# Kernel tuning notes

Hardware: AMD Instinct MI355X
Metric: run time of the kernel (lower is better)

Reference implementation:

```python
import jax, jax.numpy as jnp
import numpy as np

B, N, C, H, D, K = 8, 2000, 64, 64, 16, 2  # batch, nodes, hidden, hidden_hidden, embed_dim, cheb_k


def setup_inputs() -> dict:
    key = jax.random.key(0)
    ks = jax.random.split(key, 12)
    f = lambda k, s, sc=1.0: jax.random.normal(k, s, dtype=jnp.float32) * sc
    return {
        "z": f(ks[0], (B, N, C)),
        "W_in": f(ks[1], (H, C), 0.1),
        "b_in": f(ks[2], (H,), 0.1),
        "W_out": f(ks[3], (C * C, H), 0.05),
        "b_out": f(ks[4], (C * C,), 0.05),
        "emb": f(ks[5], (N, D), 0.1),
        "wp": f(ks[6], (D, K, H, H), 0.1),
        "bp": f(ks[7], (D, H), 0.1),
        "w1": f(ks[8], (C,)),
        "w2": f(ks[9], (C,)),
        "vs": f(ks[10], (N, N), 0.02),
        "bs": f(ks[11], (N, N), 0.02),
    }


def reference(z, W_in, b_in, W_out, b_out, emb, wp, bp, w1, w2, vs, bs):
    # linear_in + relu: (B,N,C) -> (B,N,H)
    h = jax.nn.relu(jnp.einsum("bnc,hc->bnh", z, W_in) + b_in)

    # data-adaptive graph: softmax over rows of relu(emb @ emb^T)
    A = jax.nn.softmax(jax.nn.relu(emb @ emb.T), axis=1)  # (N,N)
    S = jnp.stack([jnp.eye(N, dtype=z.dtype), A], axis=0)  # (K,N,N), cheb_k=2

    # spatial attention on h (x = h.unsqueeze(1), f_in == H == C)
    e1 = h @ w1  # (B,N)
    e2 = h @ w2  # (B,N)
    prod = e1[:, :, None] * e2[:, None, :]  # (B,N,N) outer product
    E = jax.nn.softmax(
        jnp.einsum("nm,bmp->bnp", vs, jax.nn.sigmoid(prod + bs)), axis=-1
    )  # (B,N,N)

    # batched supports: E.unsqueeze(1) @ S -> (B,K,N,N)
    sup = jnp.einsum("bnm,kmp->bknp", E, S)

    # node-adaptive weights / bias
    weights = jnp.einsum("nd,dkio->nkio", emb, wp)  # (N,K,H,H)
    bias = emb @ bp  # (N,H)

    # graph conv
    x_g = jnp.einsum("bknm,bmc->bnkc", sup, h)  # (B,N,K,H)
    g = jnp.einsum("bnki,nkio->bno", x_g, weights) + bias  # (B,N,H)

    # linear_out + view + tanh, scaled by 0.1
    out = jnp.tanh(jnp.einsum("bnh,oh->bno", g, W_out) + b_out)
    return 0.1 * out.reshape(B, N, C, C)
```

## Files before the change

kernel.cpp:

```cpp
#include <hip/hip_runtime.h>
#include <hip/hip_bf16.h>

#define NN 2000
#define NP 2048
#define BB 8
#define HH 64
#define DD 16

typedef __hip_bfloat16 bf16;
typedef short bf16x8 __attribute__((ext_vector_type(8)));
typedef float f32x4 __attribute__((ext_vector_type(4)));

__device__ __forceinline__ float fast_sigmoid(float x) {
    return 1.0f / (1.0f + __expf(-x));
}
__device__ __forceinline__ float fast_tanh(float x) {
    float e = __expf(2.0f * x);
    return 1.0f - 2.0f / (e + 1.0f);
}

__device__ __forceinline__ void glds16(const void* g, void* l) {
    __builtin_amdgcn_global_load_lds(
        (const __attribute__((address_space(1))) void*)g,
        (__attribute__((address_space(3))) void*)l, 16, 0, 0);
}

__global__ __launch_bounds__(256) void k_h(
        const float* __restrict__ z, const float* __restrict__ W_in,
        const float* __restrict__ b_in, const float* __restrict__ w1,
        const float* __restrict__ w2, float* __restrict__ h,
        float* __restrict__ e1, float* __restrict__ e2) {
    __shared__ float WT[64 * 65];
    __shared__ float zs[8][64];
    int t = threadIdx.x;
    int lane = t & 63, ty = t >> 6;
    int bn0 = blockIdx.x * 8;
    for (int i = t; i < 64 * 64; i += 256) {
        int hh = i >> 6, c = i & 63;
        WT[c * 65 + hh] = W_in[i];
    }
    #pragma unroll
    for (int q = 0; q < 2; q++) {
        int r = ty * 2 + q;
        zs[r][lane] = z[(size_t)(bn0 + r) * 64 + lane];
    }
    __syncthreads();
    #pragma unroll
    for (int q = 0; q < 2; q++) {
        int r = ty * 2 + q;
        float acc = b_in[lane];
        #pragma unroll
        for (int c = 0; c < 64; c++) acc += zs[r][c] * WT[c * 65 + lane];
        float hv = fmaxf(acc, 0.0f);
        h[(size_t)(bn0 + r) * 64 + lane] = hv;
        float p1 = hv * w1[lane], p2 = hv * w2[lane];
        #pragma unroll
        for (int off = 32; off > 0; off >>= 1) {
            p1 += __shfl_down(p1, off);
            p2 += __shfl_down(p2, off);
        }
        if (lane == 0) { e1[bn0 + r] = p1; e2[bn0 + r] = p2; }
    }
}

__global__ __launch_bounds__(256) void k_mega(
        const float* __restrict__ e1, const float* __restrict__ e2,
        const float* __restrict__ bs, bf16* __restrict__ Tt,
        const float* __restrict__ vs, bf16* __restrict__ vs_bf,
        const float* __restrict__ emb, bf16* __restrict__ A,
        const float* __restrict__ wp, float* __restrict__ Wn_all,
        const float* __restrict__ h, bf16* __restrict__ hTcat,
        bf16* __restrict__ hsT,
        const float* __restrict__ W_out, bf16* __restrict__ Wo_bf) {
    __shared__ float smem[4160];
    int bid = blockIdx.x, t = threadIdx.x;

    if (bid < 1024) {
        int mt = bid & 31, pt = bid >> 5;
        float* tile = smem;
        int tx = t & 63, ty = t >> 6;
        int m0 = mt * 64, p0 = pt * 64;
        for (int i = ty * 16; i < ty * 16 + 16; i++) {
            int m = m0 + i, p = p0 + tx;
            tile[i * 65 + tx] = (m < NN && p < NN) ? bs[(size_t)m * NN + p] : 0.0f;
        }
        __syncthreads();
        int m = m0 + tx;
        for (int b = 0; b < BB; b++) {
            float e1v = (m < NN) ? e1[b * NN + m] : 0.0f;
            bf16* Tb = Tt + (size_t)b * NP * NP;
            for (int i = ty * 16; i < ty * 16 + 16; i++) {
                int p = p0 + i;
                float v = 0.0f;
                if (m < NN && p < NN)
                    v = fast_sigmoid(e1v * e2[b * NN + p] + tile[tx * 65 + i]);
                Tb[((size_t)p) * NP + m] = __float2bfloat16(v);
            }
        }
        return;
    }
    bid -= 1024;
    if (bid < 16384) {
        int id = bid * 256 + t;
        int n = id >> 11, m = id & (NP - 1);
        float v = (n < NN && m < NN) ? vs[n * NN + m] : 0.0f;
        vs_bf[id] = __float2bfloat16(v);
        return;
    }
    bid -= 16384;
    if (bid < 2048) {
        int i = bid;
        if (i >= NN) {
            for (int j = t; j < NP; j += 256) A[(size_t)i * NP + j] = __float2bfloat16(0.0f);
            return;
        }
        float* rowbuf = smem;
        float* red = smem + 2048;
        float* ei = smem + 2304;
        if (t < DD) ei[t] = emb[i * DD + t];
        __syncthreads();
        float lmax = -1e30f;
        for (int j = t; j < NP; j += 256) {
            float s = 0.0f;
            if (j < NN) {
                #pragma unroll
                for (int d = 0; d < DD; d++) s += ei[d] * emb[j * DD + d];
                s = fmaxf(s, 0.0f);
                lmax = fmaxf(lmax, s);
            }
            rowbuf[j] = s;
        }
        red[t] = lmax; __syncthreads();
        for (int o = 128; o > 0; o >>= 1) { if (t < o) red[t] = fmaxf(red[t], red[t + o]); __syncthreads(); }
        float mx = red[0];
        __syncthreads();
        float lsum = 0.0f;
        for (int j = t; j < NN; j += 256) {
            float e = __expf(rowbuf[j] - mx);
            rowbuf[j] = e; lsum += e;
        }
        red[t] = lsum; __syncthreads();
        for (int o = 128; o > 0; o >>= 1) { if (t < o) red[t] += red[t + o]; __syncthreads(); }
        float inv = 1.0f / red[0];
        for (int j = t; j < NP; j += 256)
            A[(size_t)i * NP + j] = __float2bfloat16(j < NN ? rowbuf[j] * inv : 0.0f);
        return;
    }
    bid -= 2048;
    if (bid < 512) {
        float* embs = smem;
        int n0 = (bid & 15) * 128;
        int jo = (bid >> 4) * 256 + t;
        float wv[16];
        #pragma unroll
        for (int d = 0; d < 16; d++) wv[d] = wp[(size_t)d * 8192 + jo];
        for (int s = t; s < 128 * 16; s += 256) {
            int i = s >> 4, d = s & 15;
            int n = n0 + i;
            embs[s] = (n < NN) ? emb[n * 16 + d] : 0.f;
        }
        __syncthreads();
        for (int i = 0; i < 128; i++) {
            int n = n0 + i;
            if (n >= NN) break;
            const f32x4* ev = (const f32x4*)&embs[i * 16];
            f32x4 ea = ev[0], eb = ev[1], ec = ev[2], ed = ev[3];
            float a = 0.f;
            #pragma unroll
            for (int q = 0; q < 4; q++) a += ea[q] * wv[q];
            #pragma unroll
            for (int q = 0; q < 4; q++) a += eb[q] * wv[4 + q];
            #pragma unroll
            for (int q = 0; q < 4; q++) a += ec[q] * wv[8 + q];
            #pragma unroll
            for (int q = 0; q < 4; q++) a += ed[q] * wv[12 + q];
            Wn_all[(size_t)n * 8192 + jo] = a;
        }
        return;
    }
    bid -= 512;
    if (bid < 256) {
        float* tile = smem;
        int nt = bid & 31, b = bid >> 5;
        int tx = t & 63, ty = t >> 6;
        int n0 = nt * 64;
        for (int i = ty * 16; i < ty * 16 + 16; i++) {
            int n = n0 + i;
            tile[i * 65 + tx] = (n < NN) ? h[((size_t)b * NN + n) * 64 + tx] : 0.0f;
        }
        __syncthreads();
        for (int i = ty * 16; i < ty * 16 + 16; i++) {
            bf16 v = __float2bfloat16(tile[tx * 65 + i]);
            hTcat[((size_t)b * 64 + i) * NP + n0 + tx] = v;
            hsT[((size_t)b * 128 + i) * NP + n0 + tx] = v;
        }
        return;
    }
    bid -= 256;
    {
        int id = bid * 256 + t;
        Wo_bf[id] = __float2bfloat16(W_out[id]);
    }
}

__global__ __launch_bounds__(256) void k_redT(const float* __restrict__ AhPart,
                                              bf16* __restrict__ hsT) {
    __shared__ float tile[64 * 65];
    int pt = blockIdx.x, b = blockIdx.y;
    int tx = threadIdx.x & 63, ty = threadIdx.x >> 6;
    int p0 = pt * 64, q0 = b * 64;
    const long long TOT = (long long)NP * 512;
    for (int i = ty * 16; i < ty * 16 + 16; i++) {
        long long base = ((long long)p0 + i) * 512 + q0 + tx;
        float s = AhPart[base];
        #pragma unroll
        for (int sl = 1; sl < 4; sl++) s += AhPart[sl * TOT + base];
        tile[i * 65 + tx] = s;
    }
    __syncthreads();
    for (int i = ty * 16; i < ty * 16 + 16; i++)
        hsT[((size_t)b * 128 + 64 + i) * NP + p0 + tx] =
            __float2bfloat16(tile[tx * 65 + i]);
}

#define MFMA_B16 __builtin_amdgcn_mfma_f32_16x16x32_bf16
#define VM8 asm volatile("s_waitcnt vmcnt(8)" ::: "memory")
#define VM4 asm volatile("s_waitcnt vmcnt(4)" ::: "memory")
#define VM0 asm volatile("s_waitcnt vmcnt(0)" ::: "memory")
#define VMN
#define PHASE(BUF, KH, JP, READA, STAGE, VMS)                                \
  {                                                                          \
    if (READA) {                                                             \
      _Pragma("unroll")                                                      \
      for (int ii = 0; ii < 8; ii++)                                         \
        a[ii] = *(const bf16x8*)(LDSb + (BUF) * 16384 + (KH) * 8192 + aoff[ii]); \
    }                                                                        \
    b[0] = *(const bf16x8*)(LDSb + 32768 + (BUF) * 16384 + (KH) * 8192 + boff[(JP) * 2]); \
    b[1] = *(const bf16x8*)(LDSb + 32768 + (BUF) * 16384 + (KH) * 8192 + boff[(JP) * 2 + 1]); \
    STAGE;                                                                   \
    asm volatile("s_waitcnt lgkmcnt(0)" ::: "memory");                       \
    __builtin_amdgcn_sched_barrier(0);                                       \
    __builtin_amdgcn_s_setprio(1);                                           \
    _Pragma("unroll")                                                        \
    for (int ii = 0; ii < 8; ii++) {                                         \
      acc[ii][(JP) * 2]     = MFMA_B16(a[ii], b[0], acc[ii][(JP) * 2], 0, 0, 0);     \
      acc[ii][(JP) * 2 + 1] = MFMA_B16(a[ii], b[1], acc[ii][(JP) * 2 + 1], 0, 0, 0); \
    }                                                                        \
    __builtin_amdgcn_s_setprio(0);                                           \
    __builtin_amdgcn_sched_barrier(0);                                       \
    VMS;                                                                     \
    __builtin_amdgcn_s_barrier();                                            \
    __builtin_amdgcn_sched_barrier(0);                                       \
  }

__global__ __launch_bounds__(512, 2) void k_gemm256pv(
        const bf16* __restrict__ X, const bf16* __restrict__ Yt,
        const bf16* __restrict__ hsT, float* __restrict__ xgPart,
        float* __restrict__ rsPart,
        int K, int ldx, int ldy, long long sY, long long sHs) {
    __shared__ short LDSb[65536];
    int id = blockIdx.x;
    int xcd = id & 7;
    int bx = (id >> 3) & 7;
    int group = (id >> 6) * 8 + xcd;
    int by = group & 7, z = group >> 3;
    const bf16* Xp = X;
    const bf16* Yp = Yt + (long long)z * sY;
    int tid = threadIdx.x;
    int m0 = bx * 256, n0 = by * 256;
    int wave = tid >> 6, lane = tid & 63;
    int wr = wave >> 2, wc = wave & 3;
    int fr = lane & 15, kq = lane >> 4;

    f32x4 zero = {0.f, 0.f, 0.f, 0.f};
    f32x4 acc[8][4];
    #pragma unroll
    for (int i = 0; i < 8; i++)
        #pragma unroll
        for (int j = 0; j < 4; j++) acc[i][j] = zero;

    auto SR = [&](int isA, int buf, int kh, int tile) {
        int rbase = (isA ? 0 : 32768) + buf * 16384 + kh * 8192;
        long long kb = (long long)tile * 64 + kh * 32;
        #pragma unroll
        for (int q = 0; q < 2; q++) {
            int pos = q * 512 + tid;
            int row = pos >> 2;
            int scol = ((pos & 3) ^ (row & 3) ^ ((row >> 2) & 3)) * 8;
            const bf16* g = (isA ? Xp + (long long)(m0 + row) * ldx
                                 : Yp + (long long)(n0 + row) * ldy) + kb + scol;
            glds16(g, LDSb + rbase + pos * 8);
        }
    };

    int aoff[8], boff[4];
    #pragma unroll
    for (int i = 0; i < 8; i++) {
        int row = wr * 128 + i * 16 + fr;
        aoff[i] = row * 32 + ((kq ^ (row & 3) ^ ((row >> 2) & 3)) << 3);
    }
    #pragma unroll
    for (int j = 0; j < 4; j++) {
        int row = wc * 64 + j * 16 + fr;
        boff[j] = row * 32 + ((kq ^ (row & 3) ^ ((row >> 2) & 3)) << 3);
    }

    bf16x8 a[8], b[2];
    int NITER = K >> 7;

    SR(1, 0, 0, 0); SR(0, 0, 0, 0);
    SR(1, 0, 1, 0); SR(0, 0, 1, 0);
    SR(1, 1, 0, 1); SR(0, 1, 0, 1);
    VM8;
    __builtin_amdgcn_s_barrier();
    __builtin_amdgcn_sched_barrier(0);

    for (int i = 0; i < NITER - 1; i++) {
        int t1 = 2 * i + 1, t2 = 2 * i + 2, t3 = 2 * i + 3;
        PHASE(0, 0, 0, 1, { SR(1, 1, 1, t1); }, VM8)
        PHASE(0, 0, 1, 0, { SR(0, 1, 1, t1); }, VM8)
        PHASE(0, 1, 0, 1, { SR(1, 0, 0, t2); }, VM8)
        PHASE(0, 1, 1, 0, { SR(0, 0, 0, t2); }, VM8)
        PHASE(1, 0, 0, 1, { SR(1, 0, 1, t2); }, VM8)
        PHASE(1, 0, 1, 0, { SR(0, 0, 1, t2); }, VM8)
        PHASE(1, 1, 0, 1, { SR(1, 1, 0, t3); }, VM8)
        PHASE(1, 1, 1, 0, { SR(0, 1, 0, t3); }, VM8)
    }
    {
        int t1 = 2 * NITER - 1;
        PHASE(0, 0, 0, 1, { SR(1, 1, 1, t1); }, VM8)
        PHASE(0, 0, 1, 0, { SR(0, 1, 1, t1); }, VM8)
        PHASE(0, 1, 0, 1, { }, VM8)
        PHASE(0, 1, 1, 0, { }, VM4)
        PHASE(1, 0, 0, 1, { }, VM4)
        PHASE(1, 0, 1, 0, { }, VM0)
        PHASE(1, 1, 0, 1, { }, VMN)
        PHASE(1, 1, 1, 0, { }, VMN)
    }
    __syncthreads();

    int rq = kq * 4;
    #pragma unroll
    for (int i = 0; i < 8; i++) {
        #pragma unroll
        for (int r = 0; r < 4; r++) {
            int lrow = wr * 128 + i * 16 + rq + r;
            float rs = 0.f;
            #pragma unroll
            for (int j = 0; j < 4; j++) {
                int lcol = wc * 64 + j * 16 + fr;
                float e = (n0 + lcol < NN) ? __expf(acc[i][j][r]) : 0.f;
                bf16 bv = __float2bfloat16(e);
                int sl = (lcol >> 3) ^ (lrow & 7);
                LDSb[lrow * 256 + sl * 8 + (lcol & 7)] = *(short*)&bv;
                rs += e;
            }
            rs += __shfl_xor(rs, 1);
            rs += __shfl_xor(rs, 2);
            rs += __shfl_xor(rs, 4);
            rs += __shfl_xor(rs, 8);
            if (fr == 0)
                rsPart[((long long)z * 32 + by * 4 + wc) * NP + m0 + lrow] = rs;
        }
    }
    __syncthreads();

    const bf16* hz = hsT + (long long)z * sHs;
    int wr2 = wave >> 2, wc2 = wave & 3;
    f32x4 acc2[8][2];
    #pragma unroll
    for (int i = 0; i < 8; i++)
        #pragma unroll
        for (int jj = 0; jj < 2; jj++) acc2[i][jj] = zero;
    #pragma unroll
    for (int ks = 0; ks < 8; ks++) {
        bf16x8 a2[8], b2[2];
        #pragma unroll
        for (int i = 0; i < 8; i++) {
            int row = wr2 * 128 + i * 16 + fr;
            int sl = (ks * 4 + kq) ^ (row & 7);
            a2[i] = *(const bf16x8*)(LDSb + row * 256 + sl * 8);
        }
        #pragma unroll
        for (int jj = 0; jj < 2; jj++)
            b2[jj] = *(const bf16x8*)(hz + (long long)(wc2 * 32 + jj * 16 + fr) * NP
                                      + n0 + ks * 32 + kq * 8);
        #pragma unroll
        for (int i = 0; i < 8; i++)
            #pragma unroll
            for (int jj = 0; jj < 2; jj++)
                acc2[i][jj] = MFMA_B16(a2[i], b2[jj], acc2[i][jj], 0, 0, 0);
    }
    #pragma unroll
    for (int i = 0; i < 8; i++)
        #pragma unroll
        for (int jj = 0; jj < 2; jj++) {
            int jcol = wc2 * 32 + jj * 16 + fr;
            #pragma unroll
            for (int r = 0; r < 4; r++) {
                int n = m0 + wr2 * 128 + i * 16 + rq + r;
                xgPart[(long long)n * 8192 + by * 1024 + z * 128 + jcol] = acc2[i][jj][r];
            }
        }
}

template<bool TANH, int KSPLIT>
__global__ __launch_bounds__(256) void k_gemm_bt(
        const bf16* __restrict__ X, const bf16* __restrict__ Yt,
        float* __restrict__ C, const float* __restrict__ bias,
        int K, int ldx, int ldy, int ldc,
        long long sX, long long sY, long long sC, long long sSlice) {
    __shared__ short As[128 * 32];
    __shared__ short Bs[128 * 32];
    int zz = blockIdx.z;
    int ks = 0;
    if (KSPLIT > 1) { ks = zz % KSPLIT; zz /= KSPLIT; }
    const bf16* Xp = X + (long long)zz * sX;
    const bf16* Yp = Yt + (long long)zz * sY;
    float* Cp = C + (long long)zz * sC + (long long)ks * sSlice;
    int tid = threadIdx.x;
    int m0 = blockIdx.x * 128, n0 = blockIdx.y * 128;
    int wave = tid >> 6, lane = tid & 63;
    int wm = (wave >> 1) * 64, wn = (wave & 1) * 64;
    int fr = lane & 15, kq = lane >> 4;

    f32x4 zero = {0.f, 0.f, 0.f, 0.f};
    f32x4 acc[4][4];
    #pragma unroll
    for (int i = 0; i < 4; i++)
        #pragma unroll
        for (int j = 0; j < 4; j++) acc[i][j] = zero;

    int lrow = lane >> 2, lcol = (lane & 3) * 8;
    const bf16* xg0 = Xp + (long long)(m0 + wave * 16 + lrow) * ldx + lcol;
    const bf16* xg1 = xg0 + (long long)64 * ldx;
    const bf16* yg0 = Yp + (long long)(n0 + wave * 16 + lrow) * ldy + lcol;
    const bf16* yg1 = yg0 + (long long)64 * ldy;
    short* lA0 = As + wave * 512;
    short* lA1 = As + (wave + 4) * 512;
    short* lB0 = Bs + wave * 512;
    short* lB1 = Bs + (wave + 4) * 512;

    int kbeg = (KSPLIT > 1) ? ks * (K / KSPLIT) : 0;
    int kend = kbeg + K / KSPLIT;
    for (int k0 = kbeg; k0 < kend; k0 += 32) {
        __syncthreads();
        glds16(xg0 + k0, lA0);
        glds16(xg1 + k0, lA1);
        glds16(yg0 + k0, lB0);
        glds16(yg1 + k0, lB1);
        __syncthreads();
        bf16x8 a[4], b[4];
        #pragma unroll
        for (int i = 0; i < 4; i++)
            a[i] = *(const bf16x8*)(As + (wm + i * 16 + fr) * 32 + kq * 8);
        #pragma unroll
        for (int j = 0; j < 4; j++)
            b[j] = *(const bf16x8*)(Bs + (wn + j * 16 + fr) * 32 + kq * 8);
        #pragma unroll
        for (int i = 0; i < 4; i++)
            #pragma unroll
            for (int j = 0; j < 4; j++)
                acc[i][j] = __builtin_amdgcn_mfma_f32_16x16x32_bf16(a[i], b[j], acc[i][j], 0, 0, 0);
    }
    int rq = kq * 4;
    for (int i = 0; i < 4; i++)
        for (int j = 0; j < 4; j++) {
            int col = n0 + wn + j * 16 + fr;
            float bv = TANH ? bias[col] : 0.0f;
            #pragma unroll
            for (int r = 0; r < 4; r++) {
                int row = m0 + wm + i * 16 + rq + r;
                float v = acc[i][j][r];
                Cp[(long long)row * ldc + col] =
                    TANH ? 0.1f * fast_tanh(v + bv) : v;
            }
        }
}

__global__ __launch_bounds__(256) void k_g(
        const float* __restrict__ Wn_all, const float* __restrict__ bp,
        const float* __restrict__ emb, const float* __restrict__ xgPart,
        const float* __restrict__ rsPart, bf16* __restrict__ gbf) {
    __shared__ float Wn[8192];
    __shared__ float xgs[1024];
    __shared__ float biass[64];
    __shared__ float invs[8];
    __shared__ float rsred[256];
    int n = blockIdx.x, t = threadIdx.x;
    rsred[t] = rsPart[(size_t)t * NP + n];
    if (t >= 64 && t < 128) {
        int o = t - 64;
        float a = 0.f;
        #pragma unroll
        for (int d = 0; d < 16; d++) a += emb[n * 16 + d] * bp[d * 64 + o];
        biass[o] = a;
    }
    {
        const f32x4* src = (const f32x4*)(Wn_all + (size_t)n * 8192);
        f32x4* dst = (f32x4*)Wn;
        #pragma unroll
        for (int s = 0; s < 8; s++) dst[s * 256 + t] = src[s * 256 + t];
    }
    __syncthreads();
    if (t < 8) {
        float s = 0.f;
        #pragma unroll
        for (int y = 0; y < 32; y++) s += rsred[t * 32 + y];
        invs[t] = 1.0f / s;
    }
    __syncthreads();
    for (int s = 0; s < 4; s++) {
        int id = t + s * 256;
        int b = id >> 7, j = id & 127;
        const float* xp = xgPart + (size_t)n * 8192 + b * 128 + j;
        float a = xp[0];
        #pragma unroll
        for (int by = 1; by < 8; by++) a += xp[by * 1024];
        xgs[id] = a * invs[b];
    }
    __syncthreads();
    int o = t & 63, bh = t >> 6;
    for (int half = 0; half < 2; half++) {
        int b = bh + half * 4;
        float a = biass[o];
        for (int j = 0; j < 128; j++) a += xgs[b * 128 + j] * Wn[j * 64 + o];
        gbf[((size_t)b * NN + n) * 64 + o] = __float2bfloat16(a);
    }
}

extern "C" void kernel_launch(void* const* d_in, const int* in_sizes, int n_in,
                              void* d_out, int out_size, void* d_ws, size_t ws_size,
                              hipStream_t stream) {
    const float* z     = (const float*)d_in[0];
    const float* W_in  = (const float*)d_in[1];
    const float* b_in  = (const float*)d_in[2];
    const float* W_out = (const float*)d_in[3];
    const float* b_out = (const float*)d_in[4];
    const float* emb   = (const float*)d_in[5];
    const float* wp    = (const float*)d_in[6];
    const float* bp    = (const float*)d_in[7];
    const float* w1    = (const float*)d_in[8];
    const float* w2    = (const float*)d_in[9];
    const float* vs    = (const float*)d_in[10];
    const float* bs    = (const float*)d_in[11];

    char* p = (char*)d_ws;
    auto alloc = [&](size_t bytes) -> char* {
        char* r = p;
        p += (bytes + 255) & ~(size_t)255;
        return r;
    };
    float* h       = (float*)alloc((size_t)BB * NN * 64 * 4);
    float* e1      = (float*)alloc((size_t)BB * NN * 4);
    float* e2      = (float*)alloc((size_t)BB * NN * 4);
    bf16*  A_bf    = (bf16*) alloc((size_t)NP * NP * 2);
    bf16*  vs_bf   = (bf16*) alloc((size_t)NP * NP * 2);
    bf16*  Tt_all  = (bf16*) alloc((size_t)BB * NP * NP * 2);
    float* rsPart  = (float*)alloc((size_t)BB * 32 * NP * 4);
    bf16*  hTcat   = (bf16*) alloc((size_t)512 * NP * 2);
    float* AhPart  = (float*)alloc((size_t)4 * NP * 512 * 4);
    bf16*  hsT     = (bf16*) alloc((size_t)BB * 128 * NP * 2);
    float* xgPart  = (float*)alloc((size_t)NP * 8192 * 4);
    bf16*  gbf     = (bf16*) alloc((size_t)BB * NN * 64 * 2);
    bf16*  Wo_bf   = (bf16*) alloc((size_t)4096 * 64 * 2);
    float* Wn_all  = (float*)alloc((size_t)NN * 8192 * 4);

    k_h<<<BB * NN / 8, 256, 0, stream>>>(z, W_in, b_in, w1, w2, h, e1, e2);

    k_mega<<<1024 + 16384 + 2048 + 512 + 256 + 1024, 256, 0, stream>>>(
        e1, e2, bs, Tt_all, vs, vs_bf, emb, A_bf, wp, Wn_all,
        h, hTcat, hsT, W_out, Wo_bf);

    k_gemm_bt<false, 4><<<dim3(16, 4, 4), 256, 0, stream>>>(
        A_bf, hTcat, AhPart, nullptr, NP, NP, NP, 512,
        0, 0, 0, (long long)NP * 512);
    k_redT<<<dim3(NP / 64, BB), 256, 0, stream>>>(AhPart, hsT);

    k_gemm256pv<<<512, 512, 0, stream>>>(
        vs_bf, Tt_all, hsT, xgPart, rsPart, NP, NP, NP,
        (long long)NP * NP, (long long)128 * NP);

    k_g<<<NN, 256, 0, stream>>>(Wn_all, bp, emb, xgPart, rsPart, gbf);
    k_gemm_bt<true, 1><<<dim3(125, 32, 1), 256, 0, stream>>>(
        gbf, Wo_bf, (float*)d_out, b_out, 64, 64, 64, 4096, 0, 0, 0, 0);
}
```

Baseline: 587.3 us.

## Double-buffer A fragments to prefetch next k-slice during MFMA in GEMM main loop

The main loop of the 256x256 GEMM now loads the A-operand fragments for the next k-half into a second register set while the current MFMAs run. It also loads all four B fragments at once and waits with partial lgkmcnt counts, so LDS read latency overlaps with matrix math instead of being fully exposed each phase. The cost is eight more bf16x8 register arrays under a 512-thread, 2-wave-per-SIMD launch bound, which risks spills or lower occupancy. The ordering of A reads against the barriers and staging writes has to stay correct.

Measured after the change: 607.2 us. 1.03x slower.

```diff
diff --git a/kernel.cpp b/kernel.cpp
--- a/kernel.cpp
+++ b/kernel.cpp
@@ -228,29 +228,62 @@
 #define VM4 asm volatile("s_waitcnt vmcnt(4)" ::: "memory")
 #define VM0 asm volatile("s_waitcnt vmcnt(0)" ::: "memory")
 #define VMN
-#define PHASE(BUF, KH, JP, READA, STAGE, VMS)                                \
+#define SBAR __builtin_amdgcn_s_barrier()
+#define SCB  __builtin_amdgcn_sched_barrier(0)
+#define LDB(BUF, KH, J) \
+    (*(const bf16x8*)(LDSb + 32768 + (BUF) * 16384 + (KH) * 8192 + boff[J]))
+
+#define SPAIR(BUF, KH, NB, NK, AC, AN, S1, S2, V1, V2)                       \
+  {                                                                          \
+    bq[0] = LDB(BUF, KH, 0); bq[1] = LDB(BUF, KH, 1);                        \
+    bq[2] = LDB(BUF, KH, 2); bq[3] = LDB(BUF, KH, 3);                        \
+    S1;                                                                      \
+    asm volatile("s_waitcnt lgkmcnt(2)" ::: "memory");                       \
+    SCB;                                                                     \
+    __builtin_amdgcn_s_setprio(1);                                           \
+    _Pragma("unroll")                                                        \
+    for (int ii = 0; ii < 8; ii++) {                                         \
+      acc[ii][0] = MFMA_B16(AC[ii], bq[0], acc[ii][0], 0, 0, 0);             \
+      acc[ii][1] = MFMA_B16(AC[ii], bq[1], acc[ii][1], 0, 0, 0);             \
+    }                                                                        \
+    __builtin_amdgcn_s_setprio(0);                                           \
+    SCB; V1; SBAR; SCB;                                                      \
+    _Pragma("unroll")                                                        \
+    for (int ii = 0; ii < 8; ii++)                                           \
+      AN[ii] = *(const bf16x8*)(LDSb + (NB) * 16384 + (NK) * 8192 + aoff[ii]); \
+    S2;                                                                      \
+    asm volatile("s_waitcnt lgkmcnt(8)" ::: "memory");                       \
+    SCB;                                                                     \
+    __builtin_amdgcn_s_setprio(1);                                           \
+    _Pragma("unroll")                                                        \
+    for (int ii = 0; ii < 8; ii++) {                                         \
+      acc[ii][2] = MFMA_B16(AC[ii], bq[2], acc[ii][2], 0, 0, 0);             \
+      acc[ii][3] = MFMA_B16(AC[ii], bq[3], acc[ii][3], 0, 0, 0);             \
+    }                                                                        \
+    __builtin_amdgcn_s_setprio(0);                                           \
+    SCB; V2; SBAR; SCB;                                                      \
+  }
+
+#define FPHASE(BUF, KH, JP, READA, STAGE, VMS)                               \
   {                                                                          \
     if (READA) {                                                             \
       _Pragma("unroll")                                                      \
       for (int ii = 0; ii < 8; ii++)                                         \
-        a[ii] = *(const bf16x8*)(LDSb + (BUF) * 16384 + (KH) * 8192 + aoff[ii]); \
+        aA[ii] = *(const bf16x8*)(LDSb + (BUF) * 16384 + (KH) * 8192 + aoff[ii]); \
     }                                                                        \
-    b[0] = *(const bf16x8*)(LDSb + 32768 + (BUF) * 16384 + (KH) * 8192 + boff[(JP) * 2]); \
-    b[1] = *(const bf16x8*)(LDSb + 32768 + (BUF) * 16384 + (KH) * 8192 + boff[(JP) * 2 + 1]); \
+    bq[0] = LDB(BUF, KH, (JP) * 2);                                          \
+    bq[1] = LDB(BUF, KH, (JP) * 2 + 1);                                      \
     STAGE;                                                                   \
     asm volatile("s_waitcnt lgkmcnt(0)" ::: "memory");                       \
-    __builtin_amdgcn_sched_barrier(0);                                       \
+    SCB;                                                                     \
     __builtin_amdgcn_s_setprio(1);                                           \
     _Pragma("unroll")                                                        \
     for (int ii = 0; ii < 8; ii++) {                                         \
-      acc[ii][(JP) * 2]     = MFMA_B16(a[ii], b[0], acc[ii][(JP) * 2], 0, 0, 0);     \
-      acc[ii][(JP) * 2 + 1] = MFMA_B16(a[ii], b[1], acc[ii][(JP) * 2 + 1], 0, 0, 0); \
+      acc[ii][(JP) * 2]     = MFMA_B16(aA[ii], bq[0], acc[ii][(JP) * 2], 0, 0, 0);     \
+      acc[ii][(JP) * 2 + 1] = MFMA_B16(aA[ii], bq[1], acc[ii][(JP) * 2 + 1], 0, 0, 0); \
     }                                                                        \
     __builtin_amdgcn_s_setprio(0);                                           \
-    __builtin_amdgcn_sched_barrier(0);                                       \
-    VMS;                                                                     \
-    __builtin_amdgcn_s_barrier();                                            \
-    __builtin_amdgcn_sched_barrier(0);                                       \
+    SCB; VMS; SBAR; SCB;                                                     \
   }
 
 __global__ __launch_bounds__(512, 2) void k_gemm256pv(
@@ -305,37 +338,35 @@
         boff[j] = row * 32 + ((kq ^ (row & 3) ^ ((row >> 2) & 3)) << 3);
     }
 
-    bf16x8 a[8], b[2];
+    bf16x8 aA[8], aB[8], bq[4];
     int NITER = K >> 7;
 
     SR(1, 0, 0, 0); SR(0, 0, 0, 0);
     SR(1, 0, 1, 0); SR(0, 0, 1, 0);
     SR(1, 1, 0, 1); SR(0, 1, 0, 1);
     VM8;
-    __builtin_amdgcn_s_barrier();
-    __builtin_amdgcn_sched_barrier(0);
+    SBAR; SCB;
+    #pragma unroll
+    for (int ii = 0; ii < 8; ii++)
+        aA[ii] = *(const bf16x8*)(LDSb + aoff[ii]);
 
     for (int i = 0; i < NITER - 1; i++) {
         int t1 = 2 * i + 1, t2 = 2 * i + 2, t3 = 2 * i + 3;
-        PHASE(0, 0, 0, 1, { SR(1, 1, 1, t1); }, VM8)
-        PHASE(0, 0, 1, 0, { SR(0, 1, 1, t1); }, VM8)
-        PHASE(0, 1, 0, 1, { SR(1, 0, 0, t2); }, VM8)
-        PHASE(0, 1, 1, 0, { SR(0, 0, 0, t2); }, VM8)
-        PHASE(1, 0, 0, 1, { SR(1, 0, 1, t2); }, VM8)
-        PHASE(1, 0, 1, 0, { SR(0, 0, 1, t2); }, VM8)
-        PHASE(1, 1, 0, 1, { SR(1, 1, 0, t3); }, VM8)
-        PHASE(1, 1, 1, 0, { SR(0, 1, 0, t3); }, VM8)
+        SPAIR(0, 0, 0, 1, aA, aB, { SR(1, 1, 1, t1); }, { SR(0, 1, 1, t1); }, VM8, VM8)
+        SPAIR(0, 1, 1, 0, aB, aA, { SR(1, 0, 0, t2); }, { SR(0, 0, 0, t2); }, VM8, VM8)
+        SPAIR(1, 0, 1, 1, aA, aB, { SR(1, 0, 1, t2); }, { SR(0, 0, 1, t2); }, VM8, VM8)
+        SPAIR(1, 1, 0, 0, aB, aA, { SR(1, 1, 0, t3); }, { SR(0, 1, 0, t3); }, VM8, VM8)
     }
     {
         int t1 = 2 * NITER - 1;
-        PHASE(0, 0, 0, 1, { SR(1, 1, 1, t1); }, VM8)
-        PHASE(0, 0, 1, 0, { SR(0, 1, 1, t1); }, VM8)
-        PHASE(0, 1, 0, 1, { }, VM8)
-        PHASE(0, 1, 1, 0, { }, VM4)
-        PHASE(1, 0, 0, 1, { }, VM4)
-        PHASE(1, 0, 1, 0, { }, VM0)
-        PHASE(1, 1, 0, 1, { }, VMN)
-        PHASE(1, 1, 1, 0, { }, VMN)
+        FPHASE(0, 0, 0, 0, { SR(1, 1, 1, t1); }, VM8)
+        FPHASE(0, 0, 1, 0, { SR(0, 1, 1, t1); }, VM8)
+        FPHASE(0, 1, 0, 1, { }, VM8)
+        FPHASE(0, 1, 1, 0, { }, VM4)
+        FPHASE(1, 0, 0, 1, { }, VM4)
+        FPHASE(1, 0, 1, 0, { }, VM0)
+        FPHASE(1, 1, 0, 1, { }, VMN)
+        FPHASE(1, 1, 1, 0, { }, VMN)
     }
     __syncthreads();
 
```
